# Kernel tuning notes

Hardware: AMD Instinct MI355X
Metric: run time of the kernel (lower is better)

The kernel has to match this reference:

```python
import jax, jax.numpy as jnp
import numpy as np

PATCH = 288
DIM = 2048
SCALE = DIM ** -0.5
NUM_INSTANCE = 4
B, Q, H, W = 32, 16, 24, 12


def _layernorm(x):
    # elementwise_affine=False LayerNorm, eps=1e-5
    m = jnp.mean(x, axis=-1, keepdims=True)
    v = jnp.mean((x - m) ** 2, axis=-1, keepdims=True)
    return (x - m) / jnp.sqrt(v + 1e-5)


def _l2norm(x):
    n = jnp.sqrt(jnp.sum(x * x, axis=-1, keepdims=True))
    return x / jnp.maximum(n, 1e-12)


def _catcher(x, g, cam_embed, Wq, Wg, pos_embed):
    # x: [B,Q,C] queries; g: [B,N,C] tokens; cam_embed: [B*N//PATCH,1,C] or None
    rel_q = jnp.einsum('bqc,dc->bqd', x, Wq)
    Bg, N, C = g.shape
    G = Bg * N // PATCH
    g2 = g.reshape(G, PATCH, C)
    rel = _l2norm(g2)
    rel = jax.nn.softmax(jnp.einsum('gpc,gqc->gpq', rel, rel), axis=-1)
    g2 = jnp.einsum('gpq,gqc->gpc', rel, g2)  # [G,PATCH,C]
    if cam_embed is not None:
        rel_g = g2 + cam_embed.reshape(G, 1, C)  # cam embed replaces pos embed (as in torch)
    else:
        rel_g = g2 + pos_embed
    g_out = g2.reshape(Bg, N, C)
    rel_g = jnp.einsum('bnc,dc->bnd', rel_g.reshape(Bg, N, C), Wg)
    att = jax.nn.softmax(jnp.einsum('bqc,bnc->bqn', rel_q, rel_g) * SCALE, axis=-1)
    out = jnp.einsum('bqn,bnc->bqc', att, g_out)
    return out, att


def _deltaor(x, g, Wq, Wg):
    q = _layernorm(x)
    rel_q = jnp.einsum('bqc,dc->bqd', q, Wq)
    g = g - jnp.mean(x, axis=1, keepdims=True)
    g = _layernorm(g)
    rel_g = jnp.einsum('bnc,dc->bnd', g, Wg)
    att = jax.nn.softmax(jnp.einsum('bqc,bnc->bqn', rel_q, rel_g) * SCALE, axis=-1)
    return x + jnp.einsum('bqn,bnc->bqc', att, g)


def setup_inputs() -> dict:
    key = jax.random.key(0)
    ks = jax.random.split(key, 12)
    w_scale = DIM ** -0.5
    return {
        'x': jax.random.normal(ks[0], (B, DIM, H, W), dtype=jnp.float32),
        'cam_ids': jax.random.randint(ks[1], (B,), 1, 7),
        'sub': jax.random.randint(ks[2], (B,), 0, 2).astype(bool),
        'query_v': 0.02 * jax.random.normal(ks[3], (1, Q, DIM), dtype=jnp.float32),
        'prototype': 0.02 * jax.random.normal(ks[4], (1, 2048, DIM), dtype=jnp.float32),
        'weights': jnp.ones((1, Q, 1), dtype=jnp.float32),
        'cam_table': 0.02 * jax.random.normal(ks[5], (6, 1, DIM), dtype=jnp.float32),
        'pos_embed': 0.02 * jax.random.normal(ks[6], (1, PATCH, DIM), dtype=jnp.float32),
        'Wcq': w_scale * jax.random.normal(ks[7], (DIM, DIM), dtype=jnp.float32),
        'Wcg': w_scale * jax.random.normal(ks[8], (DIM, DIM), dtype=jnp.float32),
        'Wdq': w_scale * jax.random.normal(ks[9], (DIM, DIM), dtype=jnp.float32),
        'Wdg': w_scale * jax.random.normal(ks[10], (DIM, DIM), dtype=jnp.float32),
    }


def reference(x, cam_ids, sub, query_v, prototype, weights, cam_table, pos_embed,
              Wcq, Wcg, Wdq, Wdg):
    Bx, C, Hx, Wx = x.shape
    HW = Hx * Wx
    xs = jnp.transpose(x.reshape(Bx, C, HW), (0, 2, 1))  # [B,HW,C]
    query = jnp.broadcast_to(query_v, (Bx,) + query_v.shape[1:])
    proto = jnp.broadcast_to(prototype, (Bx,) + prototype.shape[1:])
    cam_embed = cam_table[cam_ids - 1]  # [B,1,C]

    f_rel, _ = _catcher(query, xs, cam_embed, Wcq, Wcg, pos_embed)
    f_pro = _deltaor(f_rel, proto, Wdq, Wdg)

    # training branch (P2R shares weights with Q2R)
    f_rec, _ = _catcher(f_pro, xs, cam_embed, Wcq, Wcg, pos_embed)

    G = Bx // NUM_INSTANCE
    ce = cam_embed.reshape(G, 1, NUM_INSTANCE, 1, C)
    ce = jnp.broadcast_to(ce, (G, NUM_INSTANCE, NUM_INSTANCE, 1, C)).reshape(Bx, NUM_INSTANCE, C)
    xr = xs.reshape(G, 1, NUM_INSTANCE, HW, C)
    xr = jnp.broadcast_to(xr, (G, NUM_INSTANCE, NUM_INSTANCE, HW, C)).reshape(Bx, NUM_INSTANCE * HW, C)
    # torch.cat([a[~sub], a[sub]]) == stable sort by sub (False first)
    perm = jnp.argsort(sub.astype(jnp.int32))
    ce = ce[perm]
    xr = xr[perm]
    f_cor, _ = _catcher(f_pro, xr, ce, Wcq, Wcg, pos_embed)

    f_pro = jax.nn.softmax(weights, axis=1) * f_pro
    return f_rel, f_pro, f_rec, f_cor
```

## Files before the change

### kernel.cpp

```cpp
#include <hip/hip_runtime.h>
#include <math.h>

static constexpr float SCALE = 0.022097086912079612f;

typedef __bf16 bf16x4 __attribute__((ext_vector_type(4)));
typedef __bf16 bf16x8 __attribute__((ext_vector_type(8)));
typedef float  f32x4  __attribute__((ext_vector_type(4)));

__device__ __forceinline__ float wred_sum(float v){
  #pragma unroll
  for (int o=32;o>0;o>>=1) v += __shfl_down(v,o,64);
  return v;
}
__device__ __forceinline__ float wred_max(float v){
  #pragma unroll
  for (int o=32;o>0;o>>=1) v = fmaxf(v, __shfl_down(v,o,64));
  return v;
}
__device__ __forceinline__ float block_sum(float v, float* red){
  int tid=threadIdx.x, w=tid>>6, l=tid&63, nw=(int)(blockDim.x>>6);
  v = wred_sum(v);
  __syncthreads();
  if (l==0) red[w]=v;
  __syncthreads();
  float r=0.f;
  for (int i=0;i<nw;i++) r += red[i];
  return r;
}
__device__ __forceinline__ float block_max(float v, float* red){
  int tid=threadIdx.x, w=tid>>6, l=tid&63, nw=(int)(blockDim.x>>6);
  v = wred_max(v);
  __syncthreads();
  if (l==0) red[w]=v;
  __syncthreads();
  float r=red[0];
  for (int i=1;i<nw;i++) r = fmaxf(r, red[i]);
  return r;
}

template<int MT, int NT, int WM, int WN>
__global__ __launch_bounds__(256, 2)
void gemm_nt_mfma(float* __restrict__ Cm, const float* __restrict__ Am,
                  const float* __restrict__ Bm, int M, int N, int K,
                  int lda, int ldb, int ldc, long sA, long sB, long sC,
                  float alpha, const int* __restrict__ browidx, long sBrow,
                  int KS, float* __restrict__ Part)
{
  constexpr int BM = MT*16*WM;
  constexpr int BN = NT*16*WN;
  constexpr int LDH = 40;
  constexpr int AST = (BM+31)/32;
  constexpr int BST = (BN+31)/32;
  __shared__ __bf16 Ah[BM*LDH];
  __shared__ __bf16 Al[BM*LDH];
  __shared__ __bf16 Bh[BN*LDH];
  __shared__ __bf16 Bl[BN*LDH];
  int ZZ = gridDim.z / KS;
  int z  = blockIdx.z % ZZ;
  int ks = blockIdx.z / ZZ;
  const float* A = Am + (long)z*sA;
  const float* B = Bm + (long)z*sB;
  float* C = Cm + (long)z*sC;
  const bool useB = (browidx != nullptr);
  const int* brow = useB ? (browidx + (long)z*sBrow) : nullptr;
  int Kc = ((K + KS*32 - 1) / (KS*32)) * 32;
  int kbeg = ks*Kc;
  int kend = min(K, kbeg + Kc);
  int m0 = blockIdx.y*BM, n0 = blockIdx.x*BN;
  int t = threadIdx.x;
  int srow = t>>3, skoff = (t&7)*4;

  float4 areg[AST], breg[BST];
  auto loadAB = [&](int k0){
    #pragma unroll
    for (int s=0;s<AST;++s){
      int row = srow + 32*s; int gm = m0+row;
      areg[s] = make_float4(0.f,0.f,0.f,0.f);
      if (row < BM && gm < M) areg[s] = *(const float4*)(A + (long)gm*lda + k0 + skoff);
    }
    #pragma unroll
    for (int s=0;s<BST;++s){
      int row = srow + 32*s; int gn = n0+row;
      breg[s] = make_float4(0.f,0.f,0.f,0.f);
      if (row < BN && gn < N){
        long r = useB ? (long)brow[gn] : (long)gn;
        breg[s] = *(const float4*)(B + r*ldb + k0 + skoff);
      }
    }
  };
  auto writeLDS = [&](){
    #pragma unroll
    for (int s=0;s<AST;++s){
      int row = srow + 32*s;
      if (row < BM){
        float vv[4] = {areg[s].x, areg[s].y, areg[s].z, areg[s].w};
        bf16x4 hv, lv;
        #pragma unroll
        for (int e=0;e<4;++e){
          __bf16 h = (__bf16)vv[e];
          hv[e] = h;
          lv[e] = (__bf16)(vv[e] - (float)h);
        }
        *(bf16x4*)&Ah[row*LDH + skoff] = hv;
        *(bf16x4*)&Al[row*LDH + skoff] = lv;
      }
    }
    #pragma unroll
    for (int s=0;s<BST;++s){
      int row = srow + 32*s;
      if (row < BN){
        float vv[4] = {breg[s].x, breg[s].y, breg[s].z, breg[s].w};
        bf16x4 hv, lv;
        #pragma unroll
        for (int e=0;e<4;++e){
          __bf16 h = (__bf16)vv[e];
          hv[e] = h;
          lv[e] = (__bf16)(vv[e] - (float)h);
        }
        *(bf16x4*)&Bh[row*LDH + skoff] = hv;
        *(bf16x4*)&Bl[row*LDH + skoff] = lv;
      }
    }
  };

  int lane = t & 63, wid = t >> 6;
  int wm = (WM==1) ? 0 : (wid / WN);
  int wn = wid % WN;
  int mw = wm*MT*16, nw = wn*NT*16;
  int fr = lane & 15, fq = (lane>>4)*8;

  f32x4 acc[MT][NT];
  #pragma unroll
  for (int i=0;i<MT;++i)
    #pragma unroll
    for (int j=0;j<NT;++j) acc[i][j] = (f32x4){0.f,0.f,0.f,0.f};

  if (kbeg < kend) loadAB(kbeg);
  for (int k0=kbeg; k0<kend; k0+=32){
    writeLDS();
    __syncthreads();
    if (k0+32 < kend) loadAB(k0+32);
    bf16x8 ah[MT], al[MT], bh[NT], bl[NT];
    #pragma unroll
    for (int i=0;i<MT;++i){
      ah[i] = *(const bf16x8*)&Ah[(mw+i*16+fr)*LDH + fq];
      al[i] = *(const bf16x8*)&Al[(mw+i*16+fr)*LDH + fq];
    }
    #pragma unroll
    for (int j=0;j<NT;++j){
      bh[j] = *(const bf16x8*)&Bh[(nw+j*16+fr)*LDH + fq];
      bl[j] = *(const bf16x8*)&Bl[(nw+j*16+fr)*LDH + fq];
    }
    #pragma unroll
    for (int i=0;i<MT;++i)
      #pragma unroll
      for (int j=0;j<NT;++j){
        acc[i][j] = __builtin_amdgcn_mfma_f32_16x16x32_bf16(ah[i], bh[j], acc[i][j], 0,0,0);
        acc[i][j] = __builtin_amdgcn_mfma_f32_16x16x32_bf16(ah[i], bl[j], acc[i][j], 0,0,0);
        acc[i][j] = __builtin_amdgcn_mfma_f32_16x16x32_bf16(al[i], bh[j], acc[i][j], 0,0,0);
      }
    __syncthreads();
  }
  float wf = (KS==1) ? alpha : 1.f;
  float* Cw = C; int ldw = ldc;
  if (ks > 0){ Cw = Part + ((long)(ks-1)*ZZ + z)*(long)M*N; ldw = N; }
  int er = (lane>>4)*4, ec = lane & 15;
  #pragma unroll
  for (int i=0;i<MT;++i){
    int mbase = m0 + mw + i*16 + er;
    #pragma unroll
    for (int r=0;r<4;++r){
      int mm = mbase + r;
      if (mm < M){
        long cro = (long)mm*ldw;
        #pragma unroll
        for (int j=0;j<NT;++j){
          int nn = n0 + nw + j*16 + ec;
          if (nn < N) Cw[cro + nn] = wf*acc[i][j][r];
        }
      }
    }
  }
}

__global__ __launch_bounds__(256) void k_reduce(float* __restrict__ C, const float* __restrict__ Part,
                                                long total, int S, float alpha){
  for (long i = (long)blockIdx.x*blockDim.x + threadIdx.x; i < total;
       i += (long)gridDim.x*blockDim.x){
    float v = C[i];
    for (int s=0;s<S;++s) v += Part[(long)s*total + i];
    C[i] = alpha*v;
  }
}

__global__ __launch_bounds__(256, 2) void k_pv(
    float* __restrict__ C, float* __restrict__ Part,
    const float* __restrict__ Pm, long sP, int K, int Kc,
    const float* __restrict__ G, long sG, const int* __restrict__ SB)
{
  extern __shared__ float Pl[];
  int b = blockIdx.y, ks = blockIdx.z;
  int kbeg = ks * Kc;
  int kend = min(K, kbeg + Kc);
  int len = kend - kbeg;
  int c0 = blockIdx.x*1024 + threadIdx.x*4;
  const float* Pb = Pm + (long)b*sP;
  for (int i = threadIdx.x; i < 16*len; i += 256){
    int q = i / len, kk = i - q*len;
    Pl[q*Kc + kk] = Pb[(long)q*K + kbeg + kk];
  }
  __syncthreads();
  f32x4 acc[16];
  #pragma unroll
  for (int q=0;q<16;++q) acc[q] = (f32x4){0.f,0.f,0.f,0.f};
  int kk = 0;
  while (kk < len){
    int kg = kbeg + kk;
    int seg = kg / 288;
    int row = kg - seg*288;
    int nrow = min(288 - row, len - kk);
    const float* gp = (SB ? (G + (long)SB[(b<<2)+seg]*sG) : (G + (long)b*sG))
                      + (long)row*2048 + c0;
    for (int r = 0; r < nrow; r += 4, kk += 4){
      f32x4 g0 = *(const f32x4*)(gp);
      f32x4 g1 = *(const f32x4*)(gp + 2048);
      f32x4 g2 = *(const f32x4*)(gp + 4096);
      f32x4 g3 = *(const f32x4*)(gp + 6144);
      gp += 8192;
      #pragma unroll
      for (int q=0;q<16;++q){
        f32x4 p = *(const f32x4*)&Pl[q*Kc + kk];
        acc[q] += p[0]*g0;
        acc[q] += p[1]*g1;
        acc[q] += p[2]*g2;
        acc[q] += p[3]*g3;
      }
    }
  }
  float* Cw = (ks==0) ? C : (Part + (long)(ks-1)*1048576);
  long obase = (long)b*32768 + c0;
  #pragma unroll
  for (int q=0;q<16;++q) *(f32x4*)&Cw[obase + (long)q*2048] = acc[q];
}

__global__ void k_tr(const float* __restrict__ in, float* __restrict__ out, int R, int C){
  __shared__ float tile[32][33];
  long zo = (long)blockIdx.z * R * C;
  int r0 = blockIdx.y*32, c0 = blockIdx.x*32;
  int tx = threadIdx.x, ty = threadIdx.y;
  #pragma unroll
  for (int j=0;j<32;j+=8)
    tile[ty+j][tx] = in[zo + (long)(r0+ty+j)*C + c0+tx];
  __syncthreads();
  #pragma unroll
  for (int j=0;j<32;j+=8)
    out[zo + (long)(c0+ty+j)*R + r0+tx] = tile[tx][ty+j];
}

__global__ __launch_bounds__(256) void k_rowstats(const float* __restrict__ X, long ldx, int cols,
                                                  float* __restrict__ mu, float* __restrict__ m2){
  int r = blockIdx.x;
  const float* row = X + (long)r*ldx;
  float s=0.f, s2=0.f;
  for (int c = threadIdx.x*4; c < cols; c += 1024){
    float4 v = *(const float4*)(row+c);
    s  += v.x+v.y+v.z+v.w;
    s2 += v.x*v.x+v.y*v.y+v.z*v.z+v.w*v.w;
  }
  __shared__ float red[8];
  s  = block_sum(s,  red);
  s2 = block_sum(s2, red);
  if (threadIdx.x==0){ mu[r]=s/(float)cols; m2[r]=s2; }
}

__global__ __launch_bounds__(256) void k_softmax_gram(float* __restrict__ S, const float* __restrict__ m2xs){
  int r = blockIdx.x;
  int b = r / 288, p = r % 288;
  float* row = S + (long)r * 288;
  const float* m2 = m2xs + (long)b*288;
  float rp = 1.f / fmaxf(sqrtf(m2[p]), 1e-12f);
  int tid = threadIdx.x;
  __shared__ float red[8];
  float lv[2];
  #pragma unroll
  for (int i=0;i<2;++i){
    int q = tid + i*256;
    lv[i] = (q<288) ? row[q]*rp/fmaxf(sqrtf(m2[q]),1e-12f) : -1e30f;
  }
  float mx = fmaxf(lv[0], lv[1]);
  mx = block_max(mx, red);
  float s = 0.f;
  #pragma unroll
  for (int i=0;i<2;++i){
    int q = tid + i*256;
    float e = (q<288) ? expf(lv[i]-mx) : 0.f;
    lv[i]=e; s+=e;
  }
  s = block_sum(s, red);
  float inv = 1.f/s;
  #pragma unroll
  for (int i=0;i<2;++i){ int q = tid + i*256; if (q<288) row[q]=lv[i]*inv; }
}

__global__ __launch_bounds__(256) void k_softmax_plain(float* __restrict__ X, int L){
  int r = blockIdx.x;
  float* row = X + (long)r * L;
  int tid = threadIdx.x;
  __shared__ float red[8];
  float lv[8];
  #pragma unroll
  for (int i=0;i<8;++i){ int q = tid + i*256; lv[i] = (q<L) ? row[q] : -1e30f; }
  float mx = -1e30f;
  #pragma unroll
  for (int i=0;i<8;++i) mx = fmaxf(mx, lv[i]);
  mx = block_max(mx, red);
  float s = 0.f;
  #pragma unroll
  for (int i=0;i<8;++i){ int q = tid + i*256; float e = (q<L)?expf(lv[i]-mx):0.f; lv[i]=e; s+=e; }
  s = block_sum(s, red);
  float inv = 1.f/s;
  #pragma unroll
  for (int i=0;i<8;++i){ int q = tid + i*256; if (q<L) row[q]=lv[i]*inv; }
}

__global__ __launch_bounds__(256) void k_softmax_seg(float* __restrict__ X, const float* __restrict__ CC,
                                                     const int* __restrict__ SB, float scale){
  int r = blockIdx.x; int b = r>>4;
  float* row = X + (long)r*1152;
  float bias[4];
  #pragma unroll
  for (int j=0;j<4;++j) bias[j] = scale*CC[(long)r*32 + SB[b*4+j]];
  int tid = threadIdx.x;
  __shared__ float red[8];
  float lv[5];
  #pragma unroll
  for (int i=0;i<5;++i){
    int q = tid + i*256;
    lv[i] = (q<1152) ? row[q] + bias[q/288] : -1e30f;
  }
  float mx = -1e30f;
  #pragma unroll
  for (int i=0;i<5;++i) mx = fmaxf(mx, lv[i]);
  mx = block_max(mx, red);
  float s = 0.f;
  #pragma unroll
  for (int i=0;i<5;++i){ int q = tid + i*256; float e = (q<1152)?expf(lv[i]-mx):0.f; lv[i]=e; s+=e; }
  s = block_sum(s, red);
  float inv = 1.f/s;
  #pragma unroll
  for (int i=0;i<5;++i){ int q = tid + i*256; if (q<1152) row[q]=lv[i]*inv; }
}

__global__ void k_ln_apply(const float* __restrict__ X, const float* __restrict__ mu,
                           const float* __restrict__ m2, float* __restrict__ Y){
  int r = blockIdx.y; int c = blockIdx.x*256 + threadIdx.x;
  float m = mu[r];
  float v = m2[r]*(1.f/2048.f) - m*m;
  float inv = rsqrtf(v + 1e-5f);
  long idx = (long)r*2048 + c;
  Y[idx] = (X[idx] - m)*inv;
}

__global__ void k_meanx(const float* __restrict__ frel, float* __restrict__ mx){
  int b = blockIdx.y; int c = blockIdx.x*256 + threadIdx.x;
  const float* base = frel + (long)b*16*2048 + c;
  float s=0.f;
  #pragma unroll
  for (int q=0;q<16;++q) s += base[(long)q*2048];
  mx[(long)b*2048 + c] = s * (1.f/16.f);
}

__global__ void k_sigma(const float* __restrict__ pm, const float* __restrict__ mu_p,
                        const float* __restrict__ m2_p, const float* __restrict__ mu_m,
                        const float* __restrict__ m2_m, float* __restrict__ sigma){
  int b = blockIdx.y; int n = blockIdx.x*256 + threadIdx.x;
  float mp = mu_p[n], mm = mu_m[b];
  float vp = m2_p[n]*(1.f/2048.f) - mp*mp;
  float vm = m2_m[b]*(1.f/2048.f) - mm*mm;
  float cov = pm[(long)b*2048+n]*(1.f/2048.f) - mp*mm;
  sigma[(long)b*2048+n] = sqrtf(fmaxf(vp + vm - 2.f*cov, 0.f) + 1e-5f);
}

__global__ void k_fixrow(float* __restrict__ X, const float* __restrict__ mu_row,
                         const float* __restrict__ mu_w){
  int r = blockIdx.y; int d = blockIdx.x*256 + threadIdx.x;
  X[(long)r*2048 + d] -= mu_row[r] * mu_w[d] * 2048.f;
}

__global__ __launch_bounds__(256) void k_qm(const float* __restrict__ relq2,
                                            const float* __restrict__ Mx, float* __restrict__ qm){
  int r = blockIdx.x; int b = r >> 4;
  const float* a = relq2 + (long)r*2048;
  const float* m = Mx + (long)b*2048;
  float s=0.f;
  for (int c = threadIdx.x*4; c < 2048; c += 1024){
    float4 va=*(const float4*)(a+c), vm=*(const float4*)(m+c);
    s += va.x*vm.x+va.y*vm.y+va.z*vm.z+va.w*vm.w;
  }
  __shared__ float red[8];
  s = block_sum(s, red);
  if (threadIdx.x==0) qm[r]=s;
}

__global__ __launch_bounds__(256) void k_score2(float* __restrict__ QPw, const float* __restrict__ qm,
                                                const float* __restrict__ sigma, const float* __restrict__ mu_p,
                                                float* __restrict__ W1, float* __restrict__ Wmu, float scale){
  int r = blockIdx.x; int b = r >> 4;
  float* row = QPw + (long)r*2048;
  const float* sg = sigma + (long)b*2048;
  int tid = threadIdx.x;
  __shared__ float red[8];
  float qmr = qm[r];
  float lv[8], ls[8];
  #pragma unroll
  for (int i=0;i<8;++i){
    int n = tid + i*256;
    float sgn = sg[n];
    ls[i] = sgn;
    lv[i] = scale * (row[n] - qmr) / sgn;
  }
  float mx = -1e30f;
  #pragma unroll
  for (int i=0;i<8;++i) mx = fmaxf(mx, lv[i]);
  mx = block_max(mx, red);
  float se=0.f, sw=0.f, swm=0.f;
  #pragma unroll
  for (int i=0;i<8;++i){
    int n = tid + i*256;
    float e = expf(lv[i]-mx);
    lv[i] = e; se += e;
    float wv = e/ls[i];
    sw += wv; swm += wv*mu_p[n];
  }
  se  = block_sum(se,  red);
  sw  = block_sum(sw,  red);
  swm = block_sum(swm, red);
  float inv = 1.f/se;
  #pragma unroll
  for (int i=0;i<8;++i){ int n = tid + i*256; row[n] = lv[i]*inv/ls[i]; }
  if (tid==0){ W1[r]=sw*inv; Wmu[r]=swm*inv; }
}

__global__ void k_fpro_final(const float* __restrict__ frel, const float* __restrict__ out2,
                             const float* __restrict__ meanx, const float* __restrict__ mu_m,
                             const float* __restrict__ W1, const float* __restrict__ Wmu,
                             const float* __restrict__ wsm,
                             float* __restrict__ fpro, float* __restrict__ fout){
  int r = blockIdx.y; int c = blockIdx.x*256 + threadIdx.x;
  int b = r >> 4, q = r & 15;
  long idx = (long)r*2048 + c;
  float w1 = W1[r];
  float v = frel[idx] + out2[idx] - meanx[(long)b*2048+c]*w1 - Wmu[r] + mu_m[b]*w1;
  fpro[idx] = v;
  fout[idx] = wsm[q] * v;
}

__global__ void k_camb(const float* __restrict__ cam_table, const int* __restrict__ cam_ids,
                       float* __restrict__ camb){
  int b = blockIdx.y; int c = blockIdx.x*256 + threadIdx.x;
  camb[(long)b*2048 + c] = cam_table[(long)(cam_ids[b]-1)*2048 + c];
}

__global__ void k_wsoft(const float* __restrict__ w, float* __restrict__ wsm){
  if (threadIdx.x==0){
    float mx=-1e30f;
    for (int i=0;i<16;++i) mx=fmaxf(mx,w[i]);
    float e[16], s=0.f;
    for (int i=0;i<16;++i){ e[i]=expf(w[i]-mx); s+=e[i]; }
    for (int i=0;i<16;++i) wsm[i]=e[i]/s;
  }
}

__global__ void k_perm(const void* __restrict__ subp, int* __restrict__ gidx, int* __restrict__ SB){
  __shared__ int perm[32];
  if (threadIdx.x==0){
    const int* pi = (const int*)subp;
    const float* pf = (const float*)subp;
    const unsigned char* pb = (const unsigned char*)subp;
    int sv[32]; bool okI=true, okF=true;
    for (int i=0;i<32;++i){ int v=pi[i]; if (v!=0 && v!=1) okI=false; }
    for (int i=0;i<32;++i){ float f=pf[i]; if (f!=0.f && f!=1.f) okF=false; }
    for (int i=0;i<32;++i){
      if (okI) sv[i]=pi[i];
      else if (okF) sv[i]=(pf[i]!=0.f)?1:0;
      else sv[i]=(pb[i]!=0)?1:0;
    }
    int pos=0;
    for (int i=0;i<32;++i) if (!sv[i]) perm[pos++]=i;
    for (int i=0;i<32;++i) if ( sv[i]) perm[pos++]=i;
  }
  __syncthreads();
  for (int i = threadIdx.x; i < 128; i += blockDim.x){
    int b = i>>2, j = i&3;
    SB[i] = ((perm[b]>>2)<<2) + j;
  }
  for (int idx = threadIdx.x; idx < 32*1152; idx += blockDim.x){
    int b = idx / 1152, rem = idx % 1152, j = rem / 288, n = rem % 288;
    int src = ((perm[b] >> 2) << 2) + j;
    gidx[idx] = src*288 + n;
  }
}

extern "C" void kernel_launch(void* const* d_in, const int* in_sizes, int n_in,
                              void* d_out, int out_size, void* d_ws, size_t ws_size,
                              hipStream_t stream) {
  const float* x        = (const float*)d_in[0];
  const int*   cam_ids  = (const int*)d_in[1];
  const void*  subp     = d_in[2];
  const float* query_v  = (const float*)d_in[3];
  const float* proto    = (const float*)d_in[4];
  const float* weights  = (const float*)d_in[5];
  const float* cam_tab  = (const float*)d_in[6];
  const float* Wcq      = (const float*)d_in[8];
  const float* Wcg      = (const float*)d_in[9];
  const float* Wdq      = (const float*)d_in[10];
  const float* Wdg      = (const float*)d_in[11];
  float* out = (float*)d_out;
  float* ws  = (float*)d_ws;

  size_t o = 0;
  float* XS    = ws + o; o += 18874368;
  float* WCGT  = XS;
  float* PROTOT= XS + 4194304;
  float* P     = XS + 8388608;
  float* PART  = XS + 12582912;
  float* GMIX  = ws + o; o += 18874368;
  float* S     = ws + o; o += 2654208;
  float* MU_XS = ws + o; o += 9216;
  float* M2_XS = ws + o; o += 9216;
  float* CAMB  = ws + o; o += 65536;
  float* RQ0   = ws + o; o += 32768;
  float* RQW   = ws + o; o += 32768;
  float* SREL  = ws + o; o += 147456;
  float* MU_FR = ws + o; o += 512;
  float* M2_FR = ws + o; o += 512;
  float* QLN   = ws + o; o += 1048576;
  float* RELQ2 = ws + o; o += 1048576;
  float* MEANX = ws + o; o += 65536;
  float* MU_P  = ws + o; o += 2048;
  float* M2_P  = ws + o; o += 2048;
  float* MU_M  = ws + o; o += 64;
  float* M2_M  = ws + o; o += 64;
  float* MU_W  = ws + o; o += 2048;
  float* M2_W  = ws + o; o += 2048;
  float* PM    = ws + o; o += 65536;
  float* SIGMA = ws + o; o += 65536;
  float* MX    = ws + o; o += 65536;
  float* QP    = ws + o; o += 1048576;
  float* QM    = ws + o; o += 512;
  float* W1    = ws + o; o += 512;
  float* WMU   = ws + o; o += 512;
  float* OUT2  = ws + o; o += 1048576;
  float* FPRO  = ws + o; o += 1048576;
  float* RQ2   = ws + o; o += 1048576;
  float* RQW2  = ws + o; o += 1048576;
  float* SREC  = ws + o; o += 147456;
  float* SCOR  = ws + o; o += 589824;
  float* CC    = ws + o; o += 16384;
  float* WSM   = ws + o; o += 16;
  int*   GIDX  = (int*)(ws + o); o += 36864;
  int*   SB    = (int*)(ws + o); o += 128;

  float* F_REL = out;
  float* F_PRO = out + 1048576;
  float* F_REC = out + 2097152;
  float* F_COR = out + 3145728;

  k_tr<<<dim3(9,64,32), dim3(32,8), 0, stream>>>(x, XS, 2048, 288);
  k_rowstats<<<9216, 256, 0, stream>>>(XS, 2048, 2048, MU_XS, M2_XS);
  gemm_nt_mfma<3,3,2,2><<<dim3(3,3,256), 256, 0, stream>>>(S, XS, XS, 288,288,2048,
      2048,2048,288, 589824,589824,82944, 1.f, nullptr,0, 8, GMIX);
  k_reduce<<<1024, 256, 0, stream>>>(S, GMIX, 2654208L, 7, 1.f);
  k_softmax_gram<<<9216, 256, 0, stream>>>(S, M2_XS);
  gemm_nt_mfma<3,4,2,2><<<dim3(16,3,32), 256, 0, stream>>>(GMIX, S, x, 288,2048,288,
      288,288,2048, 82944,589824,589824, 1.f, nullptr,0, 1, nullptr);
  k_tr<<<dim3(64,64,1), dim3(32,8), 0, stream>>>(Wcg, WCGT, 2048, 2048);
  k_tr<<<dim3(64,64,1), dim3(32,8), 0, stream>>>(proto, PROTOT, 2048, 2048);
  k_camb<<<dim3(8,32), 256, 0, stream>>>(cam_tab, cam_ids, CAMB);
  k_perm<<<1, 256, 0, stream>>>(subp, GIDX, SB);

  gemm_nt_mfma<1,4,1,4><<<dim3(8,1,8), 256, 0, stream>>>(RQ0, query_v, Wcq, 16,2048,2048,
      2048,2048,2048, 0,0,0, 1.f, nullptr,0, 8, PART);
  k_reduce<<<64, 256, 0, stream>>>(RQ0, PART, 32768L, 7, 1.f);
  gemm_nt_mfma<1,4,1,4><<<dim3(8,1,8), 256, 0, stream>>>(RQW, RQ0, WCGT, 16,2048,2048,
      2048,2048,2048, 0,0,0, 1.f, nullptr,0, 8, PART);
  k_reduce<<<64, 256, 0, stream>>>(RQW, PART, 32768L, 7, 1.f);
  gemm_nt_mfma<1,4,1,4><<<dim3(2,1,256), 256, 0, stream>>>(SREL, RQW, GMIX, 16,288,2048,
      2048,2048,288, 0,589824,4608, SCALE, nullptr,0, 8, PART);
  k_reduce<<<256, 256, 0, stream>>>(SREL, PART, 147456L, 7, SCALE);
  k_softmax_plain<<<512, 256, 0, stream>>>(SREL, 288);
  k_pv<<<dim3(2,32,7), 256, 16*44*4, stream>>>(F_REL, PART, SREL, 4608, 288, 44,
      GMIX, 589824, nullptr);
  k_reduce<<<1024, 256, 0, stream>>>(F_REL, PART, 1048576L, 6, 1.f);

  k_rowstats<<<512, 256, 0, stream>>>(F_REL, 2048, 2048, MU_FR, M2_FR);
  k_ln_apply<<<dim3(8,512), 256, 0, stream>>>(F_REL, MU_FR, M2_FR, QLN);
  k_meanx<<<dim3(8,32), 256, 0, stream>>>(F_REL, MEANX);
  k_rowstats<<<32,   256, 0, stream>>>(MEANX, 2048, 2048, MU_M, M2_M);
  k_rowstats<<<2048, 256, 0, stream>>>(proto, 2048, 2048, MU_P, M2_P);
  k_rowstats<<<2048, 256, 0, stream>>>(Wdg,   2048, 2048, MU_W, M2_W);
  gemm_nt_mfma<2,2,2,2><<<dim3(32,8,6), 256, 0, stream>>>(RELQ2, QLN, Wdq, 512,2048,2048,
      2048,2048,2048, 0,0,0, 1.f, nullptr,0, 6, PART);
  k_reduce<<<1024, 256, 0, stream>>>(RELQ2, PART, 1048576L, 5, 1.f);
  gemm_nt_mfma<1,4,1,4><<<dim3(8,2,8), 256, 0, stream>>>(PM, MEANX, proto, 32,2048,2048,
      2048,2048,2048, 0,0,0, 1.f, nullptr,0, 8, PART);
  k_reduce<<<256, 256, 0, stream>>>(PM, PART, 65536L, 7, 1.f);
  k_sigma<<<dim3(8,32), 256, 0, stream>>>(PM, MU_P, M2_P, MU_M, M2_M, SIGMA);
  gemm_nt_mfma<2,4,2,2><<<dim3(16,32,2), 256, 0, stream>>>(P, proto, Wdg, 2048,2048,2048,
      2048,2048,2048, 0,0,0, 1.f, nullptr,0, 2, PART);
  k_reduce<<<1024, 256, 0, stream>>>(P, PART, 4194304L, 1, 1.f);
  k_fixrow<<<dim3(8,2048), 256, 0, stream>>>(P, MU_P, MU_W);
  gemm_nt_mfma<1,4,1,4><<<dim3(8,2,8), 256, 0, stream>>>(MX, MEANX, Wdg, 32,2048,2048,
      2048,2048,2048, 0,0,0, 1.f, nullptr,0, 8, PART);
  k_reduce<<<256, 256, 0, stream>>>(MX, PART, 65536L, 7, 1.f);
  k_fixrow<<<dim3(8,32), 256, 0, stream>>>(MX, MU_M, MU_W);
  gemm_nt_mfma<2,2,2,2><<<dim3(32,8,6), 256, 0, stream>>>(QP, RELQ2, P, 512,2048,2048,
      2048,2048,2048, 0,0,0, 1.f, nullptr,0, 6, PART);
  k_reduce<<<1024, 256, 0, stream>>>(QP, PART, 1048576L, 5, 1.f);
  k_qm<<<512, 256, 0, stream>>>(RELQ2, MX, QM);
  k_score2<<<512, 256, 0, stream>>>(QP, QM, SIGMA, MU_P, W1, WMU, SCALE);
  gemm_nt_mfma<2,2,2,2><<<dim3(32,8,6), 256, 0, stream>>>(OUT2, QP, PROTOT, 512,2048,2048,
      2048,2048,2048, 0,0,0, 1.f, nullptr,0, 6, PART);
  k_reduce<<<1024, 256, 0, stream>>>(OUT2, PART, 1048576L, 5, 1.f);
  k_wsoft<<<1, 64, 0, stream>>>(weights, WSM);
  k_fpro_final<<<dim3(8,512), 256, 0, stream>>>(F_REL, OUT2, MEANX, MU_M, W1, WMU, WSM,
                                                FPRO, F_PRO);

  gemm_nt_mfma<2,2,2,2><<<dim3(32,8,6), 256, 0, stream>>>(RQ2, FPRO, Wcq, 512,2048,2048,
      2048,2048,2048, 0,0,0, 1.f, nullptr,0, 6, PART);
  k_reduce<<<1024, 256, 0, stream>>>(RQ2, PART, 1048576L, 5, 1.f);
  gemm_nt_mfma<2,2,2,2><<<dim3(32,8,6), 256, 0, stream>>>(RQW2, RQ2, WCGT, 512,2048,2048,
      2048,2048,2048, 0,0,0, 1.f, nullptr,0, 6, PART);
  k_reduce<<<1024, 256, 0, stream>>>(RQW2, PART, 1048576L, 5, 1.f);
  gemm_nt_mfma<1,4,1,4><<<dim3(2,1,256), 256, 0, stream>>>(SREC, RQW2, GMIX, 16,288,2048,
      2048,2048,288, 32768,589824,4608, SCALE, nullptr,0, 8, PART);
  k_reduce<<<256, 256, 0, stream>>>(SREC, PART, 147456L, 7, SCALE);
  k_softmax_plain<<<512, 256, 0, stream>>>(SREC, 288);
  k_pv<<<dim3(2,32,7), 256, 16*44*4, stream>>>(F_REC, PART, SREC, 4608, 288, 44,
      GMIX, 589824, nullptr);
  k_reduce<<<1024, 256, 0, stream>>>(F_REC, PART, 1048576L, 6, 1.f);

  gemm_nt_mfma<1,4,1,4><<<dim3(1,32,8), 256, 0, stream>>>(CC, RQW2, CAMB, 512,32,2048,
      2048,2048,32, 0,0,0, 1.f, nullptr,0, 8, PART);
  k_reduce<<<64, 256, 0, stream>>>(CC, PART, 16384L, 7, 1.f);
  gemm_nt_mfma<1,4,1,4><<<dim3(5,1,128), 256, 0, stream>>>(SCOR, RQW2, GMIX, 16,1152,2048,
      2048,2048,1152, 32768,0,18432, SCALE, GIDX,1152, 4, PART);
  k_reduce<<<512, 256, 0, stream>>>(SCOR, PART, 589824L, 3, SCALE);
  k_softmax_seg<<<512, 256, 0, stream>>>(SCOR, CC, SB, SCALE);
  k_pv<<<dim3(2,32,7), 256, 16*168*4, stream>>>(F_COR, PART, SCOR, 18432, 1152, 168,
      GMIX, 589824, SB);
  k_reduce<<<1024, 256, 0, stream>>>(F_COR, PART, 1048576L, 6, 1.f);
}
```

Before: 1.105 ms.

## Replace split-K partial buffers and reduce kernels with atomicAdd into zeroed outputs

Split-K GEMM and PV kernels now accumulate straight into the destination with float atomicAdd instead of writing partial slabs that separate k_reduce launches sum afterwards. The workspace is reorganised so every atomically accumulated buffer sits in one contiguous region, zeroed with a single memset along with the output. The proto×Wdg GEMM moves from 2 to 4 K-splits. This removes about twenty reduce launches and their partial-buffer traffic, at the cost of atomic contention, extra memsets and non-deterministic summation order.

```diff
diff --git a/kernel.cpp b/kernel.cpp
--- a/kernel.cpp
+++ b/kernel.cpp
@@ -44,7 +44,7 @@
                   const float* __restrict__ Bm, int M, int N, int K,
                   int lda, int ldb, int ldc, long sA, long sB, long sC,
                   float alpha, const int* __restrict__ browidx, long sBrow,
-                  int KS, float* __restrict__ Part)
+                  int KS)
 {
   constexpr int BM = MT*16*WM;
   constexpr int BN = NT*16*WN;
@@ -161,40 +161,46 @@
       }
     __syncthreads();
   }
-  float wf = (KS==1) ? alpha : 1.f;
-  float* Cw = C; int ldw = ldc;
-  if (ks > 0){ Cw = Part + ((long)(ks-1)*ZZ + z)*(long)M*N; ldw = N; }
   int er = (lane>>4)*4, ec = lane & 15;
-  #pragma unroll
-  for (int i=0;i<MT;++i){
-    int mbase = m0 + mw + i*16 + er;
-    #pragma unroll
-    for (int r=0;r<4;++r){
-      int mm = mbase + r;
-      if (mm < M){
-        long cro = (long)mm*ldw;
-        #pragma unroll
-        for (int j=0;j<NT;++j){
-          int nn = n0 + nw + j*16 + ec;
-          if (nn < N) Cw[cro + nn] = wf*acc[i][j][r];
+  if (KS == 1){
+    #pragma unroll
+    for (int i=0;i<MT;++i){
+      int mbase = m0 + mw + i*16 + er;
+      #pragma unroll
+      for (int r=0;r<4;++r){
+        int mm = mbase + r;
+        if (mm < M){
+          long cro = (long)mm*ldc;
+          #pragma unroll
+          for (int j=0;j<NT;++j){
+            int nn = n0 + nw + j*16 + ec;
+            if (nn < N) C[cro + nn] = alpha*acc[i][j][r];
+          }
         }
       }
     }
-  }
-}
-
-__global__ __launch_bounds__(256) void k_reduce(float* __restrict__ C, const float* __restrict__ Part,
-                                                long total, int S, float alpha){
-  for (long i = (long)blockIdx.x*blockDim.x + threadIdx.x; i < total;
-       i += (long)gridDim.x*blockDim.x){
-    float v = C[i];
-    for (int s=0;s<S;++s) v += Part[(long)s*total + i];
-    C[i] = alpha*v;
+  } else {
+    #pragma unroll
+    for (int i=0;i<MT;++i){
+      int mbase = m0 + mw + i*16 + er;
+      #pragma unroll
+      for (int r=0;r<4;++r){
+        int mm = mbase + r;
+        if (mm < M){
+          long cro = (long)mm*ldc;
+          #pragma unroll
+          for (int j=0;j<NT;++j){
+            int nn = n0 + nw + j*16 + ec;
+            if (nn < N) atomicAdd(&C[cro + nn], alpha*acc[i][j][r]);
+          }
+        }
+      }
+    }
   }
 }
 
 __global__ __launch_bounds__(256, 2) void k_pv(
-    float* __restrict__ C, float* __restrict__ Part,
+    float* __restrict__ C,
     const float* __restrict__ Pm, long sP, int K, int Kc,
     const float* __restrict__ G, long sG, const int* __restrict__ SB)
 {
@@ -237,10 +243,13 @@
       }
     }
   }
-  float* Cw = (ks==0) ? C : (Part + (long)(ks-1)*1048576);
   long obase = (long)b*32768 + c0;
   #pragma unroll
-  for (int q=0;q<16;++q) *(f32x4*)&Cw[obase + (long)q*2048] = acc[q];
+  for (int q=0;q<16;++q){
+    #pragma unroll
+    for (int e=0;e<4;++e)
+      atomicAdd(&C[obase + (long)q*2048 + e], acc[q][e]);
+  }
 }
 
 __global__ void k_tr(const float* __restrict__ in, float* __restrict__ out, int R, int C){
@@ -519,23 +528,32 @@
   float* ws  = (float*)d_ws;
 
   size_t o = 0;
+  float* S     = ws + o; o += 2654208;
+  float* RQ0   = ws + o; o += 32768;
+  float* RQW   = ws + o; o += 32768;
+  float* SREL  = ws + o; o += 147456;
+  float* RELQ2 = ws + o; o += 1048576;
+  float* PM    = ws + o; o += 65536;
+  float* MX    = ws + o; o += 65536;
+  float* QP    = ws + o; o += 1048576;
+  float* OUT2  = ws + o; o += 1048576;
+  float* RQ2   = ws + o; o += 1048576;
+  float* RQW2  = ws + o; o += 1048576;
+  float* SREC  = ws + o; o += 147456;
+  float* CC    = ws + o; o += 16384;
+  float* SCOR  = ws + o; o += 589824;
+  size_t zlen = o;
   float* XS    = ws + o; o += 18874368;
   float* WCGT  = XS;
   float* PROTOT= XS + 4194304;
   float* P     = XS + 8388608;
-  float* PART  = XS + 12582912;
   float* GMIX  = ws + o; o += 18874368;
-  float* S     = ws + o; o += 2654208;
   float* MU_XS = ws + o; o += 9216;
   float* M2_XS = ws + o; o += 9216;
   float* CAMB  = ws + o; o += 65536;
-  float* RQ0   = ws + o; o += 32768;
-  float* RQW   = ws + o; o += 32768;
-  float* SREL  = ws + o; o += 147456;
   float* MU_FR = ws + o; o += 512;
   float* M2_FR = ws + o; o += 512;
   float* QLN   = ws + o; o += 1048576;
-  float* RELQ2 = ws + o; o += 1048576;
   float* MEANX = ws + o; o += 65536;
   float* MU_P  = ws + o; o += 2048;
   float* M2_P  = ws + o; o += 2048;
@@ -543,20 +561,11 @@
   float* M2_M  = ws + o; o += 64;
   float* MU_W  = ws + o; o += 2048;
   float* M2_W  = ws + o; o += 2048;
-  float* PM    = ws + o; o += 65536;
   float* SIGMA = ws + o; o += 65536;
-  float* MX    = ws + o; o += 65536;
-  float* QP    = ws + o; o += 1048576;
   float* QM    = ws + o; o += 512;
   float* W1    = ws + o; o += 512;
   float* WMU   = ws + o; o += 512;
-  float* OUT2  = ws + o; o += 1048576;
   float* FPRO  = ws + o; o += 1048576;
-  float* RQ2   = ws + o; o += 1048576;
-  float* RQW2  = ws + o; o += 1048576;
-  float* SREC  = ws + o; o += 147456;
-  float* SCOR  = ws + o; o += 589824;
-  float* CC    = ws + o; o += 16384;
   float* WSM   = ws + o; o += 16;
   int*   GIDX  = (int*)(ws + o); o += 36864;
   int*   SB    = (int*)(ws + o); o += 128;
@@ -566,32 +575,31 @@
   float* F_REC = out + 2097152;
   float* F_COR = out + 3145728;
 
+  hipMemsetAsync(ws, 0, zlen*sizeof(float), stream);
+  hipMemsetAsync(d_out, 0, (size_t)out_size, stream);
+
   k_tr<<<dim3(9,64,32), dim3(32,8), 0, stream>>>(x, XS, 2048, 288);
   k_rowstats<<<9216, 256, 0, stream>>>(XS, 2048, 2048, MU_XS, M2_XS);
   gemm_nt_mfma<3,3,2,2><<<dim3(3,3,256), 256, 0, stream>>>(S, XS, XS, 288,288,2048,
-      2048,2048,288, 589824,589824,82944, 1.f, nullptr,0, 8, GMIX);
-  k_reduce<<<1024, 256, 0, stream>>>(S, GMIX, 2654208L, 7, 1.f);
+      2048,2048,288, 589824,589824,82944, 1.f, nullptr,0, 8);
+  hipMemsetAsync(P, 0, 4194304*sizeof(float), stream);
   k_softmax_gram<<<9216, 256, 0, stream>>>(S, M2_XS);
   gemm_nt_mfma<3,4,2,2><<<dim3(16,3,32), 256, 0, stream>>>(GMIX, S, x, 288,2048,288,
-      288,288,2048, 82944,589824,589824, 1.f, nullptr,0, 1, nullptr);
+      288,288,2048, 82944,589824,589824, 1.f, nullptr,0, 1);
   k_tr<<<dim3(64,64,1), dim3(32,8), 0, stream>>>(Wcg, WCGT, 2048, 2048);
   k_tr<<<dim3(64,64,1), dim3(32,8), 0, stream>>>(proto, PROTOT, 2048, 2048);
   k_camb<<<dim3(8,32), 256, 0, stream>>>(cam_tab, cam_ids, CAMB);
   k_perm<<<1, 256, 0, stream>>>(subp, GIDX, SB);
 
   gemm_nt_mfma<1,4,1,4><<<dim3(8,1,8), 256, 0, stream>>>(RQ0, query_v, Wcq, 16,2048,2048,
-      2048,2048,2048, 0,0,0, 1.f, nullptr,0, 8, PART);
-  k_reduce<<<64, 256, 0, stream>>>(RQ0, PART, 32768L, 7, 1.f);
+      2048,2048,2048, 0,0,0, 1.f, nullptr,0, 8);
   gemm_nt_mfma<1,4,1,4><<<dim3(8,1,8), 256, 0, stream>>>(RQW, RQ0, WCGT, 16,2048,2048,
-      2048,2048,2048, 0,0,0, 1.f, nullptr,0, 8, PART);
-  k_reduce<<<64, 256, 0, stream>>>(RQW, PART, 32768L, 7, 1.f);
+      2048,2048,2048, 0,0,0, 1.f, nullptr,0, 8);
   gemm_nt_mfma<1,4,1,4><<<dim3(2,1,256), 256, 0, stream>>>(SREL, RQW, GMIX, 16,288,2048,
-      2048,2048,288, 0,589824,4608, SCALE, nullptr,0, 8, PART);
-  k_reduce<<<256, 256, 0, stream>>>(SREL, PART, 147456L, 7, SCALE);
+      2048,2048,288, 0,589824,4608, SCALE, nullptr,0, 8);
   k_softmax_plain<<<512, 256, 0, stream>>>(SREL, 288);
-  k_pv<<<dim3(2,32,7), 256, 16*44*4, stream>>>(F_REL, PART, SREL, 4608, 288, 44,
+  k_pv<<<dim3(2,32,7), 256, 16*44*4, stream>>>(F_REL, SREL, 4608, 288, 44,
       GMIX, 589824, nullptr);
-  k_reduce<<<1024, 256, 0, stream>>>(F_REL, PART, 1048576L, 6, 1.f);
 
   k_rowstats<<<512, 256, 0, stream>>>(F_REL, 2048, 2048, MU_FR, M2_FR);
   k_ln_apply<<<dim3(8,512), 256, 0, stream>>>(F_REL, MU_FR, M2_FR, QLN);
@@ -600,54 +608,41 @@
   k_rowstats<<<2048, 256, 0, stream>>>(proto, 2048, 2048, MU_P, M2_P);
   k_rowstats<<<2048, 256, 0, stream>>>(Wdg,   2048, 2048, MU_W, M2_W);
   gemm_nt_mfma<2,2,2,2><<<dim3(32,8,6), 256, 0, stream>>>(RELQ2, QLN, Wdq, 512,2048,2048,
-      2048,2048,2048, 0,0,0, 1.f, nullptr,0, 6, PART);
-  k_reduce<<<1024, 256, 0, stream>>>(RELQ2, PART, 1048576L, 5, 1.f);
+      2048,2048,2048, 0,0,0, 1.f, nullptr,0, 6);
   gemm_nt_mfma<1,4,1,4><<<dim3(8,2,8), 256, 0, stream>>>(PM, MEANX, proto, 32,2048,2048,
-      2048,2048,2048, 0,0,0, 1.f, nullptr,0, 8, PART);
-  k_reduce<<<256, 256, 0, stream>>>(PM, PART, 65536L, 7, 1.f);
+      2048,2048,2048, 0,0,0, 1.f, nullptr,0, 8);
   k_sigma<<<dim3(8,32), 256, 0, stream>>>(PM, MU_P, M2_P, MU_M, M2_M, SIGMA);
-  gemm_nt_mfma<2,4,2,2><<<dim3(16,32,2), 256, 0, stream>>>(P, proto, Wdg, 2048,2048,2048,
-      2048,2048,2048, 0,0,0, 1.f, nullptr,0, 2, PART);
-  k_reduce<<<1024, 256, 0, stream>>>(P, PART, 4194304L, 1, 1.f);
+  gemm_nt_mfma<2,4,2,2><<<dim3(16,32,4), 256, 0, stream>>>(P, proto, Wdg, 2048,2048,2048,
+      2048,2048,2048, 0,0,0, 1.f, nullptr,0, 4);
   k_fixrow<<<dim3(8,2048), 256, 0, stream>>>(P, MU_P, MU_W);
   gemm_nt_mfma<1,4,1,4><<<dim3(8,2,8), 256, 0, stream>>>(MX, MEANX, Wdg, 32,2048,2048,
-      2048,2048,2048, 0,0,0, 1.f, nullptr,0, 8, PART);
-  k_reduce<<<256, 256, 0, stream>>>(MX, PART, 65536L, 7, 1.f);
+      2048,2048,2048, 0,0,0, 1.f, nullptr,0, 8);
   k_fixrow<<<dim3(8,32), 256, 0, stream>>>(MX, MU_M, MU_W);
   gemm_nt_mfma<2,2,2,2><<<dim3(32,8,6), 256, 0, stream>>>(QP, RELQ2, P, 512,2048,2048,
-      2048,2048,2048, 0,0,0, 1.f, nullptr,0, 6, PART);
-  k_reduce<<<1024, 256, 0, stream>>>(QP, PART, 1048576L, 5, 1.f);
+      2048,2048,2048, 0,0,0, 1.f, nullptr,0, 6);
   k_qm<<<512, 256, 0, stream>>>(RELQ2, MX, QM);
   k_score2<<<512, 256, 0, stream>>>(QP, QM, SIGMA, MU_P, W1, WMU, SCALE);
   gemm_nt_mfma<2,2,2,2><<<dim3(32,8,6), 256, 0, stream>>>(OUT2, QP, PROTOT, 512,2048,2048,
-      2048,2048,2048, 0,0,0, 1.f, nullptr,0, 6, PART);
-  k_reduce<<<1024, 256, 0, stream>>>(OUT2, PART, 1048576L, 5, 1.f);
+      2048,2048,2048, 0,0,0, 1.f, nullptr,0, 6);
   k_wsoft<<<1, 64, 0, stream>>>(weights, WSM);
   k_fpro_final<<<dim3(8,512), 256, 0, stream>>>(F_REL, OUT2, MEANX, MU_M, W1, WMU, WSM,
                                                 FPRO, F_PRO);
 
   gemm_nt_mfma<2,2,2,2><<<dim3(32,8,6), 256, 0, stream>>>(RQ2, FPRO, Wcq, 512,2048,2048,
-      2048,2048,2048, 0,0,0, 1.f, nullptr,0, 6, PART);
-  k_reduce<<<1024, 256, 0, stream>>>(RQ2, PART, 1048576L, 5, 1.f);
+      2048,2048,2048, 0,0,0, 1.f, nullptr,0, 6);
   gemm_nt_mfma<2,2,2,2><<<dim3(32,8,6), 256, 0, stream>>>(RQW2, RQ2, WCGT, 512,2048,2048,
-      2048,2048,2048, 0,0,0, 1.f, nullptr,0, 6, PART);
-  k_reduce<<<1024, 256, 0, stream>>>(RQW2, PART, 1048576L, 5, 1.f);
+      2048,2048,2048, 0,0,0, 1.f, nullptr,0, 6);
   gemm_nt_mfma<1,4,1,4><<<dim3(2,1,256), 256, 0, stream>>>(SREC, RQW2, GMIX, 16,288,2048,
-      2048,2048,288, 32768,589824,4608, SCALE, nullptr,0, 8, PART);
-  k_reduce<<<256, 256, 0, stream>>>(SREC, PART, 147456L, 7, SCALE);
+      2048,2048,288, 32768,589824,4608, SCALE, nullptr,0, 8);
   k_softmax_plain<<<512, 256, 0, stream>>>(SREC, 288);
-  k_pv<<<dim3(2,32,7), 256, 16*44*4, stream>>>(F_REC, PART, SREC, 4608, 288, 44,
+  k_pv<<<dim3(2,32,7), 256, 16*44*4, stream>>>(F_REC, SREC, 4608, 288, 44,
       GMIX, 589824, nullptr);
-  k_reduce<<<1024, 256, 0, stream>>>(F_REC, PART, 1048576L, 6, 1.f);
 
   gemm_nt_mfma<1,4,1,4><<<dim3(1,32,8), 256, 0, stream>>>(CC, RQW2, CAMB, 512,32,2048,
-      2048,2048,32, 0,0,0, 1.f, nullptr,0, 8, PART);
-  k_reduce<<<64, 256, 0, stream>>>(CC, PART, 16384L, 7, 1.f);
+      2048,2048,32, 0,0,0, 1.f, nullptr,0, 8);
   gemm_nt_mfma<1,4,1,4><<<dim3(5,1,128), 256, 0, stream>>>(SCOR, RQW2, GMIX, 16,1152,2048,
-      2048,2048,1152, 32768,0,18432, SCALE, GIDX,1152, 4, PART);
-  k_reduce<<<512, 256, 0, stream>>>(SCOR, PART, 589824L, 3, SCALE);
+      2048,2048,1152, 32768,0,18432, SCALE, GIDX,1152, 4);
   k_softmax_seg<<<512, 256, 0, stream>>>(SCOR, CC, SB, SCALE);
-  k_pv<<<dim3(2,32,7), 256, 16*168*4, stream>>>(F_COR, PART, SCOR, 18432, 1152, 168,
+  k_pv<<<dim3(2,32,7), 256, 16*168*4, stream>>>(F_COR, SCOR, 18432, 1152, 168,
       GMIX, 589824, SB);
-  k_reduce<<<1024, 256, 0, stream>>>(F_COR, PART, 1048576L, 6, 1.f);
-}
+}
```

Result: slower. 1.289 ms (+16.6%).
